# Kernel optimization log

Hardware: AMD Instinct MI355X
Metric: run time of the kernel (lower is better)

## Reference

```python
import jax, jax.numpy as jnp
import numpy as np

L, S, N, E = 1024, 1024, 16, 1024

def setup_inputs() -> dict:
    key = jax.random.key(0)
    ks = jax.random.split(key, 7)
    return {
        "query": jax.random.normal(ks[0], (L, N, E), dtype=jnp.float32),
        "key": jax.random.normal(ks[1], (S, N, E), dtype=jnp.float32),
        "value": jax.random.normal(ks[2], (S, N, E), dtype=jnp.float32),
        "q_proj_weight": jax.random.normal(ks[3], (E, E), dtype=jnp.float32) * (E ** -0.5),
        "k_proj_weight": jax.random.normal(ks[4], (E, E), dtype=jnp.float32) * (E ** -0.5),
        "v_proj_weight": jax.random.normal(ks[5], (E, E), dtype=jnp.float32) * (E ** -0.5),
        "in_proj_bias": jax.random.normal(ks[6], (3 * E,), dtype=jnp.float32) * 0.02,
    }

def reference(query, key, value, q_proj_weight, k_proj_weight, v_proj_weight, in_proj_bias):
    # query: (L, N, E); key/value: (S, N, E); single head => head_dim = E
    e = query.shape[-1]
    scaling = jnp.asarray(e, query.dtype) ** -0.5
    # F.linear(x, W, b) = x @ W.T + b
    q = (jnp.einsum("lne,fe->lnf", query, q_proj_weight) + in_proj_bias[:e]) * scaling
    k = jnp.einsum("sne,fe->snf", key, k_proj_weight) + in_proj_bias[e:2 * e]
    v = jnp.einsum("sne,fe->snf", value, v_proj_weight) + in_proj_bias[2 * e:]
    # scores: (N, L, S)
    scores = jnp.einsum("lne,sne->nls", q, k)
    attn = jax.nn.softmax(scores, axis=-1)
    # output back to (L, N, E)
    out = jnp.einsum("nls,sne->lne", attn, v)
    return out
```

## Files before the change

kernel.cpp:

```cpp
#include <hip/hip_runtime.h>
#include <stdint.h>


typedef __attribute__((ext_vector_type(8))) short bf16x8;
typedef __attribute__((ext_vector_type(4))) float f32x4;

__device__ __forceinline__ float bf2f(unsigned short u) {
    union { unsigned int i; float f; } w; w.i = ((unsigned int)u) << 16; return w.f;
}
__device__ __forceinline__ unsigned short f2bf(float f) {
    union { float f; unsigned int i; } w; w.f = f;
    unsigned int r = (w.i + 0x7FFFu + ((w.i >> 16) & 1u)) >> 16;
    return (unsigned short)r;
}

__device__ __forceinline__ void g2l16(const unsigned short* g, unsigned short* l) {
    __builtin_amdgcn_global_load_lds(
        (const __attribute__((address_space(1))) unsigned int*)g,
        (__attribute__((address_space(3))) unsigned int*)l, 16, 0, 0);
}

#define BM 256
#define BN 256
#define BK 32

template <int BIAS_MODE, typename OutT>
__global__ __launch_bounds__(1024, 4) void gemm_bt2(
    const unsigned short* __restrict__ A,
    const unsigned short* __restrict__ B,
    OutT* __restrict__ C,
    const float* __restrict__ bias,
    float scale, int K,
    long lda, long ldb, long ldc,
    long aBatch, long bBatch, long cBatch,
    int gridM, int gridN)
{
    __shared__ __align__(16) unsigned short lds[65536];

    const int tid  = threadIdx.x;
    const int wave = tid >> 6;
    const int lane = tid & 63;
    const int lr   = lane & 15;
    const int q4   = lane >> 4;
    const int wm   = wave >> 2;
    const int wn   = wave & 3;

    const int p    = blockIdx.x;
    const int l    = ((p & 7) << 5) + (p >> 3);
    const int bcol = l % gridN;
    const int t2   = l / gridN;
    const int brow = t2 % gridM;
    const int bz   = t2 / gridM;

    const long m0 = (long)brow * BM;
    const long n0 = (long)bcol * BN;
    A += (long)bz * aBatch;
    B += (long)bz * bBatch;
    C += (long)bz * cBatch;

    const int tswz  = tid ^ ((tid >> 3) & 7);
    const int srow  = tswz >> 2;
    const int skoff = (tswz & 3) * 8;
    const unsigned short* aS = A + (m0 + srow) * lda + skoff;
    const unsigned short* bS = B + (n0 + srow) * ldb + skoff;
    const int ldsW = wave * 512;

    const int myoff = (((lr << 2) | q4) ^ ((lr >> 1) & 7)) << 3;

    f32x4 acc[4][4];
    const f32x4 zero = {0.f, 0.f, 0.f, 0.f};
#pragma unroll
    for (int m = 0; m < 4; m++)
#pragma unroll
        for (int n = 0; n < 4; n++) acc[m][n] = zero;

    const int nkt = K / BK;

#pragma unroll
    for (int t = 0; t < 3; t++) {
        const long kb = (long)t * BK;
        unsigned short* base = &lds[t * 16384];
        g2l16(aS + kb, base + ldsW);
        g2l16(bS + kb, base + 8192 + ldsW);
    }
    asm volatile("s_waitcnt vmcnt(4)" ::: "memory");
    __builtin_amdgcn_sched_barrier(0);
    __builtin_amdgcn_s_barrier();

    for (int kt = 0; kt < nkt; kt++) {
        const int buf  = kt & 3;
        const int sbuf = (kt + 3) & 3;
        const int st   = (kt + 3 < nkt) ? kt + 3 : nkt - 1;
        const long kb  = (long)st * BK;
        const unsigned short* At = &lds[buf * 16384];
        const unsigned short* Bt = At + 8192;
        unsigned short* sb = &lds[sbuf * 16384];

        g2l16(aS + kb, sb + ldsW);
        g2l16(bS + kb, sb + 8192 + ldsW);

        bf16x8 af[4], bfr[4];
#pragma unroll
        for (int m = 0; m < 4; m++)
            af[m] = *(const bf16x8*)&At[(wm * 64 + m * 16) * 32 + myoff];
#pragma unroll
        for (int n = 0; n < 4; n++)
            bfr[n] = *(const bf16x8*)&Bt[(wn * 64 + n * 16) * 32 + myoff];

        __builtin_amdgcn_s_setprio(1);
#pragma unroll
        for (int m = 0; m < 4; m++)
#pragma unroll
            for (int n = 0; n < 4; n++)
                acc[m][n] = __builtin_amdgcn_mfma_f32_16x16x32_bf16(
                    af[m], bfr[n], acc[m][n], 0, 0, 0);
        __builtin_amdgcn_s_setprio(0);

        asm volatile("s_waitcnt vmcnt(4)" ::: "memory");
        __builtin_amdgcn_sched_barrier(0);
        __builtin_amdgcn_s_barrier();
    }

    asm volatile("s_waitcnt vmcnt(0)" ::: "memory");
    __syncthreads();

    if constexpr (sizeof(OutT) == 2) {
#pragma unroll
        for (int m = 0; m < 4; m++)
#pragma unroll
            for (int n = 0; n < 4; n++) {
                const int col = wn * 64 + n * 16 + lr;
#pragma unroll
                for (int r = 0; r < 4; r++) {
                    const int row = wm * 64 + m * 16 + q4 * 4 + r;
                    float v = acc[m][n][r];
                    if constexpr (BIAS_MODE == 1) v += bias[n0 + col];
                    if constexpr (BIAS_MODE == 2) v += bias[m0 + row];
                    v *= scale;
                    lds[row * 256 + (col ^ (((row >> 2) & 3) << 4))] = f2bf(v);
                }
            }
        __syncthreads();
#pragma unroll
        for (int i = 0; i < 8; i++) {
            const int g   = i * 1024 + tid;
            const int row = g >> 5;
            const int ch  = g & 31;
            bf16x8 v = *(const bf16x8*)&lds[row * 256 + ((ch * 8) ^ (((row >> 2) & 3) << 4))];
            *(bf16x8*)((unsigned short*)C + (m0 + row) * ldc + n0 + ch * 8) = v;
        }
    } else {
        float* fl = (float*)lds;
#pragma unroll
        for (int h = 0; h < 2; h++) {
            __syncthreads();
            if ((wm >> 1) == h) {
#pragma unroll
                for (int m = 0; m < 4; m++)
#pragma unroll
                    for (int n = 0; n < 4; n++) {
                        const int col = wn * 64 + n * 16 + lr;
#pragma unroll
                        for (int r = 0; r < 4; r++) {
                            const int rowh = (wm & 1) * 64 + m * 16 + q4 * 4 + r;
                            float v = acc[m][n][r];
                            if constexpr (BIAS_MODE == 1) v += bias[n0 + col];
                            if constexpr (BIAS_MODE == 2) v += bias[m0 + h * 128 + rowh];
                            v *= scale;
                            fl[rowh * 256 + (col ^ (((rowh >> 2) & 3) << 4))] = v;
                        }
                    }
            }
            __syncthreads();
#pragma unroll
            for (int i = 0; i < 8; i++) {
                const int g   = i * 1024 + tid;
                const int row = g >> 6;
                const int ch  = g & 63;
                float4 v = *(const float4*)&fl[row * 256 + ((ch * 4) ^ (((row >> 2) & 3) << 4))];
                *(float4*)((float*)C + (m0 + h * 128 + row) * ldc + n0 + ch * 4) = v;
            }
        }
    }
}

__global__ __launch_bounds__(256) void cvt2_f32_bf16(
    const float* __restrict__ inA, unsigned short* __restrict__ outA, long n8A,
    const float* __restrict__ inB, unsigned short* __restrict__ outB, long n8B)
{
    const long total  = n8A + n8B;
    const long stride = (long)gridDim.x * blockDim.x;
    for (long i = (long)blockIdx.x * blockDim.x + threadIdx.x; i < total; i += stride) {
        const float* src;
        unsigned short* dst;
        long j;
        if (i < n8A) { src = inA; dst = outA; j = i; }
        else         { src = inB; dst = outB; j = i - n8A; }
        const float4* pp = (const float4*)(src + j * 8);
        float4 a = pp[0], b = pp[1];
        bf16x8 v;
        v[0] = (short)f2bf(a.x); v[1] = (short)f2bf(a.y);
        v[2] = (short)f2bf(a.z); v[3] = (short)f2bf(a.w);
        v[4] = (short)f2bf(b.x); v[5] = (short)f2bf(b.y);
        v[6] = (short)f2bf(b.z); v[7] = (short)f2bf(b.w);
        *(bf16x8*)(dst + j * 8) = v;
    }
}

__global__ __launch_bounds__(256) void softmax_rows(unsigned short* __restrict__ base)
{
    unsigned short* p = base + (long)blockIdx.x * 1024;
    const int tid = threadIdx.x;
    ushort4 u = ((const ushort4*)p)[tid];
    float x0 = bf2f(u.x), x1 = bf2f(u.y), x2 = bf2f(u.z), x3 = bf2f(u.w);
    x0 = fminf(fmaxf(x0, -1e30f), 1e30f);
    x1 = fminf(fmaxf(x1, -1e30f), 1e30f);
    x2 = fminf(fmaxf(x2, -1e30f), 1e30f);
    x3 = fminf(fmaxf(x3, -1e30f), 1e30f);

    float m = fmaxf(fmaxf(x0, x1), fmaxf(x2, x3));
#pragma unroll
    for (int o = 32; o > 0; o >>= 1) m = fmaxf(m, __shfl_xor(m, o));
    __shared__ float redm[4], reds[4];
    const int wave = tid >> 6, lane = tid & 63;
    if (lane == 0) redm[wave] = m;
    __syncthreads();
    m = fmaxf(fmaxf(redm[0], redm[1]), fmaxf(redm[2], redm[3]));

    float e0 = __expf(x0 - m), e1 = __expf(x1 - m);
    float e2 = __expf(x2 - m), e3 = __expf(x3 - m);
    float s = e0 + e1 + e2 + e3;
#pragma unroll
    for (int o = 32; o > 0; o >>= 1) s += __shfl_xor(s, o);
    if (lane == 0) reds[wave] = s;
    __syncthreads();
    s = reds[0] + reds[1] + reds[2] + reds[3];
    const float inv = 1.0f / s;

    ushort4 ov = make_ushort4(f2bf(e0 * inv), f2bf(e1 * inv),
                              f2bf(e2 * inv), f2bf(e3 * inv));
    ((ushort4*)p)[tid] = ov;
}

extern "C" void kernel_launch(void* const* d_in, const int* in_sizes, int n_in,
                              void* d_out, int out_size, void* d_ws, size_t ws_size,
                              hipStream_t stream) {
    const float* query = (const float*)d_in[0];
    const float* keyp  = (const float*)d_in[1];
    const float* valp  = (const float*)d_in[2];
    const float* wq    = (const float*)d_in[3];
    const float* wk    = (const float*)d_in[4];
    const float* wv    = (const float*)d_in[5];
    const float* bias  = (const float*)d_in[6];
    float* out = (float*)d_out;

    unsigned short* WSA = (unsigned short*)d_ws;
    unsigned short* WSB = WSA + 16777216;
    unsigned short* OC  = (unsigned short*)d_out;
    unsigned short* OD  = OC + 16777216;

    const dim3 cblk(256, 1, 1);
    const dim3 gblk(1024, 1, 1);

    cvt2_f32_bf16<<<2048, cblk, 0, stream>>>(query, WSA, 2097152, wq, WSB, 131072);
    gemm_bt2<1, unsigned short><<<256, gblk, 0, stream>>>(
        WSA, WSB, OC, bias, 0.03125f, 1024,
        1024, 1024, 1024, 0, 0, 0, 64, 4);
    cvt2_f32_bf16<<<2048, cblk, 0, stream>>>(keyp, WSA, 2097152, wk, WSB, 131072);
    gemm_bt2<1, unsigned short><<<256, gblk, 0, stream>>>(
        WSA, WSB, OD, bias + 1024, 1.0f, 1024,
        1024, 1024, 1024, 0, 0, 0, 64, 4);
    gemm_bt2<0, unsigned short><<<256, gblk, 0, stream>>>(
        OC, OD, WSB, nullptr, 1.0f, 1024,
        16384, 16384, 1024, 1024, 1024, 1048576, 4, 4);
    softmax_rows<<<16384, cblk, 0, stream>>>(WSB);
    cvt2_f32_bf16<<<2048, cblk, 0, stream>>>(valp, OC, 2097152, wv, OD, 131072);
    gemm_bt2<2, unsigned short><<<256, gblk, 0, stream>>>(
        OD, OC, WSA, bias + 2048, 1.0f, 1024,
        1024, 16384, 1024, 0, 1024, 1048576, 4, 4);
    gemm_bt2<0, float><<<256, gblk, 0, stream>>>(
        WSB, WSA, out, nullptr, 1.0f, 1024,
        1024, 1024, 16384, 1048576, 1048576, 1024, 4, 4);
}
```

Before: 425.7 us.

## Merge conversion kernels and switch softmax to one wave per row

Combines the query, key and all three weight conversions into one launch over a flat block range. Value conversion becomes a simple non-grid-stride kernel. Buffer assignments are reshuffled so all weights live in one bf16 region, and softmax now gives each 1024-wide row to a single wave. The softmax change removes the LDS reductions and __syncthreads and uses 16-byte loads and stores. The aim is fewer launches and less sync and address overhead in the memory-bound conversion and softmax passes, at the cost of tighter buffer aliasing across stages.

Measured after the change: 422.5 us. About the same (-0.7%).

```diff
diff --git a/kernel.cpp b/kernel.cpp
--- a/kernel.cpp
+++ b/kernel.cpp
@@ -184,62 +184,82 @@
     }
 }
 
-__global__ __launch_bounds__(256) void cvt2_f32_bf16(
-    const float* __restrict__ inA, unsigned short* __restrict__ outA, long n8A,
-    const float* __restrict__ inB, unsigned short* __restrict__ outB, long n8B)
+__global__ __launch_bounds__(256) void cvt_all(
+    const float* __restrict__ q,  unsigned short* __restrict__ qb,
+    const float* __restrict__ k,  unsigned short* __restrict__ kb,
+    const float* __restrict__ wq, const float* __restrict__ wk,
+    const float* __restrict__ wv, unsigned short* __restrict__ wb)
 {
-    const long total  = n8A + n8B;
-    const long stride = (long)gridDim.x * blockDim.x;
-    for (long i = (long)blockIdx.x * blockDim.x + threadIdx.x; i < total; i += stride) {
-        const float* src;
-        unsigned short* dst;
-        long j;
-        if (i < n8A) { src = inA; dst = outA; j = i; }
-        else         { src = inB; dst = outB; j = i - n8A; }
-        const float4* pp = (const float4*)(src + j * 8);
-        float4 a = pp[0], b = pp[1];
-        bf16x8 v;
-        v[0] = (short)f2bf(a.x); v[1] = (short)f2bf(a.y);
-        v[2] = (short)f2bf(a.z); v[3] = (short)f2bf(a.w);
-        v[4] = (short)f2bf(b.x); v[5] = (short)f2bf(b.y);
-        v[6] = (short)f2bf(b.z); v[7] = (short)f2bf(b.w);
-        *(bf16x8*)(dst + j * 8) = v;
-    }
-}
-
-__global__ __launch_bounds__(256) void softmax_rows(unsigned short* __restrict__ base)
+    const int b = blockIdx.x;
+    const float* src;
+    unsigned short* dst;
+    long item;
+    if (b < 8192)       { src = q; dst = qb; item = (long)b * 256 + threadIdx.x; }
+    else if (b < 16384) { src = k; dst = kb; item = (long)(b - 8192) * 256 + threadIdx.x; }
+    else {
+        const int wsel = (b - 16384) >> 9;
+        src = (wsel == 0) ? wq : ((wsel == 1) ? wk : wv);
+        dst = wb + (long)wsel * 1048576;
+        item = (long)((b - 16384) & 511) * 256 + threadIdx.x;
+    }
+    const float4* pp = (const float4*)(src + item * 8);
+    float4 a = pp[0], c = pp[1];
+    bf16x8 v;
+    v[0] = (short)f2bf(a.x); v[1] = (short)f2bf(a.y);
+    v[2] = (short)f2bf(a.z); v[3] = (short)f2bf(a.w);
+    v[4] = (short)f2bf(c.x); v[5] = (short)f2bf(c.y);
+    v[6] = (short)f2bf(c.z); v[7] = (short)f2bf(c.w);
+    *(bf16x8*)(dst + item * 8) = v;
+}
+
+__global__ __launch_bounds__(256) void cvt_one(
+    const float* __restrict__ in, unsigned short* __restrict__ out)
 {
-    unsigned short* p = base + (long)blockIdx.x * 1024;
-    const int tid = threadIdx.x;
-    ushort4 u = ((const ushort4*)p)[tid];
-    float x0 = bf2f(u.x), x1 = bf2f(u.y), x2 = bf2f(u.z), x3 = bf2f(u.w);
-    x0 = fminf(fmaxf(x0, -1e30f), 1e30f);
-    x1 = fminf(fmaxf(x1, -1e30f), 1e30f);
-    x2 = fminf(fmaxf(x2, -1e30f), 1e30f);
-    x3 = fminf(fmaxf(x3, -1e30f), 1e30f);
-
-    float m = fmaxf(fmaxf(x0, x1), fmaxf(x2, x3));
+    const long item = (long)blockIdx.x * 256 + threadIdx.x;
+    const float4* pp = (const float4*)(in + item * 8);
+    float4 a = pp[0], c = pp[1];
+    bf16x8 v;
+    v[0] = (short)f2bf(a.x); v[1] = (short)f2bf(a.y);
+    v[2] = (short)f2bf(a.z); v[3] = (short)f2bf(a.w);
+    v[4] = (short)f2bf(c.x); v[5] = (short)f2bf(c.y);
+    v[6] = (short)f2bf(c.z); v[7] = (short)f2bf(c.w);
+    *(bf16x8*)(out + item * 8) = v;
+}
+
+__global__ __launch_bounds__(256) void softmax_wave(unsigned short* __restrict__ base)
+{
+    const int wave = threadIdx.x >> 6, lane = threadIdx.x & 63;
+    unsigned short* p = base + ((long)blockIdx.x * 4 + wave) * 1024;
+
+    bf16x8 v0 = *(const bf16x8*)(p + lane * 8);
+    bf16x8 v1 = *(const bf16x8*)(p + 512 + lane * 8);
+    float x[16];
+#pragma unroll
+    for (int i = 0; i < 8; i++) {
+        x[i]     = fminf(fmaxf(bf2f((unsigned short)v0[i]), -1e30f), 1e30f);
+        x[8 + i] = fminf(fmaxf(bf2f((unsigned short)v1[i]), -1e30f), 1e30f);
+    }
+    float m = x[0];
+#pragma unroll
+    for (int i = 1; i < 16; i++) m = fmaxf(m, x[i]);
 #pragma unroll
     for (int o = 32; o > 0; o >>= 1) m = fmaxf(m, __shfl_xor(m, o));
-    __shared__ float redm[4], reds[4];
-    const int wave = tid >> 6, lane = tid & 63;
-    if (lane == 0) redm[wave] = m;
-    __syncthreads();
-    m = fmaxf(fmaxf(redm[0], redm[1]), fmaxf(redm[2], redm[3]));
-
-    float e0 = __expf(x0 - m), e1 = __expf(x1 - m);
-    float e2 = __expf(x2 - m), e3 = __expf(x3 - m);
-    float s = e0 + e1 + e2 + e3;
+
+    float e[16], s = 0.f;
+#pragma unroll
+    for (int i = 0; i < 16; i++) { e[i] = __expf(x[i] - m); s += e[i]; }
 #pragma unroll
     for (int o = 32; o > 0; o >>= 1) s += __shfl_xor(s, o);
-    if (lane == 0) reds[wave] = s;
-    __syncthreads();
-    s = reds[0] + reds[1] + reds[2] + reds[3];
     const float inv = 1.0f / s;
 
-    ushort4 ov = make_ushort4(f2bf(e0 * inv), f2bf(e1 * inv),
-                              f2bf(e2 * inv), f2bf(e3 * inv));
-    ((ushort4*)p)[tid] = ov;
+    bf16x8 o0, o1;
+#pragma unroll
+    for (int i = 0; i < 8; i++) {
+        o0[i] = (short)f2bf(e[i] * inv);
+        o1[i] = (short)f2bf(e[8 + i] * inv);
+    }
+    *(bf16x8*)(p + lane * 8) = o0;
+    *(bf16x8*)(p + 512 + lane * 8) = o1;
 }
 
 extern "C" void kernel_launch(void* const* d_in, const int* in_sizes, int n_in,
@@ -262,21 +282,20 @@
     const dim3 cblk(256, 1, 1);
     const dim3 gblk(1024, 1, 1);
 
-    cvt2_f32_bf16<<<2048, cblk, 0, stream>>>(query, WSA, 2097152, wq, WSB, 131072);
+    cvt_all<<<17920, cblk, 0, stream>>>(query, WSA, keyp, WSB, wq, wk, wv, OD);
     gemm_bt2<1, unsigned short><<<256, gblk, 0, stream>>>(
-        WSA, WSB, OC, bias, 0.03125f, 1024,
+        WSA, OD, OC, bias, 0.03125f, 1024,
         1024, 1024, 1024, 0, 0, 0, 64, 4);
-    cvt2_f32_bf16<<<2048, cblk, 0, stream>>>(keyp, WSA, 2097152, wk, WSB, 131072);
     gemm_bt2<1, unsigned short><<<256, gblk, 0, stream>>>(
-        WSA, WSB, OD, bias + 1024, 1.0f, 1024,
+        WSB, OD + 1048576, WSA, bias + 1024, 1.0f, 1024,
         1024, 1024, 1024, 0, 0, 0, 64, 4);
     gemm_bt2<0, unsigned short><<<256, gblk, 0, stream>>>(
-        OC, OD, WSB, nullptr, 1.0f, 1024,
+        OC, WSA, WSB, nullptr, 1.0f, 1024,
         16384, 16384, 1024, 1024, 1024, 1048576, 4, 4);
-    softmax_rows<<<16384, cblk, 0, stream>>>(WSB);
-    cvt2_f32_bf16<<<2048, cblk, 0, stream>>>(valp, OC, 2097152, wv, OD, 131072);
+    softmax_wave<<<4096, cblk, 0, stream>>>(WSB);
+    cvt_one<<<8192, cblk, 0, stream>>>(valp, OC);
     gemm_bt2<2, unsigned short><<<256, gblk, 0, stream>>>(
-        OD, OC, WSA, bias + 2048, 1.0f, 1024,
+        OD + 2097152, OC, WSA, bias + 2048, 1.0f, 1024,
         1024, 16384, 1024, 0, 1024, 1048576, 4, 4);
     gemm_bt2<0, float><<<256, gblk, 0, stream>>>(
         WSB, WSA, out, nullptr, 1.0f, 1024,
```
